# Kernel tuning notes

Measured on AMD Instinct MI355X. Metric: run time of the kernel, lower is better.

Reference implementation:

```python
import jax, jax.numpy as jnp
import numpy as np

HID = 128
NUM_LAYERS = 3
B = 256
ND, ED, SD = 16384, 65536, 131072
NP_, EP, SP = 131072, 524288, 524288


def setup_inputs():
    key = jax.random.key(0)
    ks = jax.random.split(key, 40)
    r = lambda i, sh: jax.random.normal(ks[i], sh, jnp.float32) * 0.05
    ri = lambda i, sh, hi: jax.random.randint(ks[i], sh, 0, hi, jnp.int32)
    return {
        'drug_x': r(0, (ND, 78)),
        'prot_x': r(1, (NP_, 70)),
        'd_feature': r(2, (B, HID)),
        'p_feature': r(3, (B, HID)),
        'drug_edge_index': ri(4, (2, ED), ND),
        'drug_batch': jnp.sort(ri(5, (ND,), B)),
        'drug_sub_node': ri(6, (SD,), ND),
        'drug_sub_ind': ri(7, (SD,), ND),
        'prot_edge_index': ri(8, (2, EP), NP_),
        'prot_batch': jnp.sort(ri(9, (NP_,), B)),
        'prot_sub_node': ri(10, (SP,), NP_),
        'prot_sub_ind': ri(11, (SP,), NP_),
        'enc_Wd': r(12, (78, HID)), 'enc_bd': r(13, (HID,)),
        'enc_Wp': r(14, (70, HID)), 'enc_bp': r(15, (HID,)),
        'convW_d': r(16, (NUM_LAYERS, HID, HID)), 'convb_d': r(17, (NUM_LAYERS, HID)),
        'convW_p': r(18, (NUM_LAYERS, HID, HID)), 'convb_p': r(19, (NUM_LAYERS, HID)),
        'bng_d': jnp.ones((NUM_LAYERS, HID), jnp.float32), 'bnb_d': jnp.zeros((NUM_LAYERS, HID), jnp.float32),
        'bng_p': jnp.ones((NUM_LAYERS, HID), jnp.float32), 'bnb_p': jnp.zeros((NUM_LAYERS, HID), jnp.float32),
        'vn_emb_d': r(20, (HID,)), 'vn_emb_p': r(21, (HID,)),
        'vnW_d': r(22, (NUM_LAYERS - 1, HID, HID)), 'vnb_d': r(23, (NUM_LAYERS - 1, HID)),
        'vnW_p': r(24, (NUM_LAYERS - 1, HID, HID)), 'vnb_p': r(25, (NUM_LAYERS - 1, HID)),
        'mlpd1_W': r(26, (2 * HID, HID)), 'mlpd1_b': r(27, (HID,)),
        'mlpd1_g': jnp.ones((HID,), jnp.float32), 'mlpd1_be': jnp.zeros((HID,), jnp.float32),
        'mlpp1_W': r(28, (2 * HID, HID)), 'mlpp1_b': r(29, (HID,)),
        'mlpp1_g': jnp.ones((HID,), jnp.float32), 'mlpp1_be': jnp.zeros((HID,), jnp.float32),
    }


def _bn(x, g, b):
    # training-mode batch norm (batch statistics)
    m = jnp.mean(x, 0)
    v = jnp.var(x, 0)
    return (x - m) * jax.lax.rsqrt(v + 1e-5) * g + b


def _seg_mean(x, ids, n):
    s = jax.ops.segment_sum(x, ids, num_segments=n)
    c = jax.ops.segment_sum(jnp.ones((x.shape[0],), x.dtype), ids, num_segments=n)
    return s / jnp.maximum(c, 1.0)[:, None]


def _gcn(h, W, b, ei, n):
    # PyG GCNConv: sym-normalized A+I, then linear
    src, dst = ei[0], ei[1]
    hw = h @ W
    deg = jax.ops.segment_sum(jnp.ones((src.shape[0],), h.dtype), dst, num_segments=n) + 1.0
    nrm = jax.lax.rsqrt(deg)
    msg = hw[src] * (nrm[src] * nrm[dst])[:, None]  # [E, HID]
    return jax.ops.segment_sum(msg, dst, num_segments=n) + hw * (nrm * nrm)[:, None] + b


def _forward(fl, ints):
    (drug_x, prot_x, d_feature, p_feature, enc_Wd, enc_bd, enc_Wp, enc_bp,
     convW_d, convb_d, convW_p, convb_p, bng_d, bnb_d, bng_p, bnb_p,
     vn_emb_d, vn_emb_p, vnW_d, vnb_d, vnW_p, vnb_p,
     mlpd1_W, mlpd1_b, mlpd1_g, mlpd1_be, mlpp1_W, mlpp1_b, mlpp1_g, mlpp1_be) = fl
    (d_ei, d_batch, d_sn, d_si, p_ei, p_batch, p_sn, p_si) = ints
    Nd, Npn = drug_x.shape[0], prot_x.shape[0]
    Bn = d_feature.shape[0]
    hd = drug_x @ enc_Wd + enc_bd
    hp = prot_x @ enc_Wp + enc_bp
    # virtual node init: learned embedding + pretrained fingerprint feature
    vx_d = vn_emb_d[None, :] + d_feature  # [B, HID]
    vx_p = vn_emb_p[None, :] + p_feature
    for i in range(NUM_LAYERS):
        # virtual-node broadcast -> GCN -> BN -> ReLU (dropout off / eval)
        hd = _gcn(hd + vx_d[d_batch], convW_d[i], convb_d[i], d_ei, Nd)
        hp = _gcn(hp + vx_p[p_batch], convW_p[i], convb_p[i], p_ei, Npn)
        hd = jax.nn.relu(_bn(hd, bng_d[i], bnb_d[i]))
        hp = jax.nn.relu(_bn(hp, bng_p[i], bnb_p[i]))
        # k-hop subgraph structure extraction (scatter_mean back to nodes)
        hd_struct = _seg_mean(hd[d_sn], d_si, Nd)
        hp_struct = _seg_mean(hp[p_sn], p_si, Npn)
        if i < NUM_LAYERS - 1:
            vx_d = vx_d + jax.nn.relu((jax.ops.segment_sum(hd_struct, d_batch, num_segments=Bn) + vx_d) @ vnW_d[i] + vnb_d[i])
            vx_p = vx_p + jax.nn.relu((jax.ops.segment_sum(hp_struct, p_batch, num_segments=Bn) + vx_p) @ vnW_p[i] + vnb_p[i])
    # cross-modal sync: broadcast pooled drug info onto protein nodes & vice versa
    sync_drug = hp_struct + _seg_mean(hd_struct, d_batch, Bn)[p_batch]  # [Np, HID]
    sync_prot = hd_struct + _seg_mean(hp_struct, p_batch, Bn)[d_batch]  # [Nd, HID]
    final_drug = _bn(jnp.concatenate([_seg_mean(sync_prot, d_batch, Bn), d_feature], 1) @ mlpd1_W + mlpd1_b, mlpd1_g, mlpd1_be)
    final_prot = _bn(jnp.concatenate([_seg_mean(sync_drug, p_batch, Bn), p_feature], 1) @ mlpp1_W + mlpp1_b, mlpp1_g, mlpp1_be)
    return final_drug, final_prot


def reference(drug_x, prot_x, d_feature, p_feature, drug_edge_index, drug_batch,
              drug_sub_node, drug_sub_ind, prot_edge_index, prot_batch,
              prot_sub_node, prot_sub_ind, enc_Wd, enc_bd, enc_Wp, enc_bp,
              convW_d, convb_d, convW_p, convb_p, bng_d, bnb_d, bng_p, bnb_p,
              vn_emb_d, vn_emb_p, vnW_d, vnb_d, vnW_p, vnb_p,
              mlpd1_W, mlpd1_b, mlpd1_g, mlpd1_be, mlpp1_W, mlpp1_b, mlpp1_g, mlpp1_be):
    fl = (drug_x, prot_x, d_feature, p_feature, enc_Wd, enc_bd, enc_Wp, enc_bp,
          convW_d, convb_d, convW_p, convb_p, bng_d, bnb_d, bng_p, bnb_p,
          vn_emb_d, vn_emb_p, vnW_d, vnb_d, vnW_p, vnb_p,
          mlpd1_W, mlpd1_b, mlpd1_g, mlpd1_be, mlpp1_W, mlpp1_b, mlpp1_g, mlpp1_be)
    ints = (drug_edge_index, drug_batch, drug_sub_node, drug_sub_ind,
            prot_edge_index, prot_batch, prot_sub_node, prot_sub_ind)
    return _forward(fl, ints)
```

## Files before the change

### kernel.cpp

```cpp
#include <hip/hip_runtime.h>
#include <cstdint>
#include <cstddef>

#define HID 128

using bf16x8 = __attribute__((ext_vector_type(8))) short;
using f32x4v = __attribute__((ext_vector_type(4))) float;

static __device__ __forceinline__ unsigned short f2b(float x) {
  unsigned int u = __float_as_uint(x);
  unsigned int r = u + 0x7FFFu + ((u >> 16) & 1u);
  return (unsigned short)(r >> 16);
}
static __device__ __forceinline__ float b2f(unsigned short h) {
  return __uint_as_float(((unsigned int)h) << 16);
}

static __device__ __forceinline__ int lowerb(const int* __restrict__ a, int n, int v) {
  int lo = 0, hi = n;
  while (lo < hi) { int m = (lo + hi) >> 1; if (a[m] < v) lo = m + 1; else hi = m; }
  return lo;
}

__global__ void k_hist_all(const int* i0, int n0, int* c0, const int* i1, int n1, int* c1,
                           const int* i2, int n2, int* c2, const int* i3, int n3, int* c3) {
  const int seg = blockIdx.x & 3;
  const int lb = blockIdx.x >> 2;
  const int stride = (gridDim.x >> 2) * blockDim.x;
  const int start = lb * blockDim.x + threadIdx.x;
  const int* idx = seg == 0 ? i0 : seg == 1 ? i1 : seg == 2 ? i2 : i3;
  int* cnt = seg == 0 ? c0 : seg == 1 ? c1 : seg == 2 ? c2 : c3;
  const int n = seg == 0 ? n0 : seg == 1 ? n1 : seg == 2 ? n2 : n3;
  for (int i = start; i < n; i += stride) atomicAdd(&cnt[idx[i]], 1);
}

__global__ void k_nrm_nb(const int* __restrict__ deg_d, float* __restrict__ nrm_d, int ND,
                         const int* __restrict__ deg_p, float* __restrict__ nrm_p, int NP,
                         const int* __restrict__ d_batch, float* __restrict__ nb_d,
                         const int* __restrict__ p_batch, float* __restrict__ nb_p, int B) {
  const int stride = gridDim.x * blockDim.x;
  const int total = ND + NP + 2 * B;
  for (int i = blockIdx.x * blockDim.x + threadIdx.x; i < total; i += stride) {
    if (i < ND) nrm_d[i] = rsqrtf((float)deg_d[i] + 1.0f);
    else if (i < ND + NP) { const int j = i - ND; nrm_p[j] = rsqrtf((float)deg_p[j] + 1.0f); }
    else if (i < ND + NP + B) {
      const int b = i - ND - NP;
      nb_d[b] = (float)(lowerb(d_batch, ND, b + 1) - lowerb(d_batch, ND, b));
    } else {
      const int b = i - ND - NP - B;
      nb_p[b] = (float)(lowerb(p_batch, NP, b + 1) - lowerb(p_batch, NP, b));
    }
  }
}

__global__ __launch_bounds__(256)
void k_scan1_all(const int* c0, int* r0, int n0, int nb0,
                 const int* c1, int* r1, int n1, int nb1,
                 const int* c2, int* r2, int n2, int nb2,
                 const int* c3, int* r3, int n3, int nb3, int* aux) {
  __shared__ int sh[256];
  int b = blockIdx.x, seg = 0;
  if (b >= nb0) { b -= nb0; seg = 1; }
  if (seg == 1 && b >= nb1) { b -= nb1; seg = 2; }
  if (seg == 2 && b >= nb2) { b -= nb2; seg = 3; }
  const int* cnt = seg == 0 ? c0 : seg == 1 ? c1 : seg == 2 ? c2 : c3;
  int* row = seg == 0 ? r0 : seg == 1 ? r1 : seg == 2 ? r2 : r3;
  const int n = seg == 0 ? n0 : seg == 1 ? n1 : seg == 2 ? n2 : n3;
  const int tid = threadIdx.x;
  const int base = b * 1024 + tid * 4;
  int v0 = base + 0 < n ? cnt[base + 0] : 0;
  int v1 = base + 1 < n ? cnt[base + 1] : 0;
  int v2 = base + 2 < n ? cnt[base + 2] : 0;
  int v3 = base + 3 < n ? cnt[base + 3] : 0;
  const int s = v0 + v1 + v2 + v3;
  sh[tid] = s;
  __syncthreads();
  for (int o = 1; o < 256; o <<= 1) {
    const int t = (tid >= o) ? sh[tid - o] : 0;
    __syncthreads();
    sh[tid] += t;
    __syncthreads();
  }
  int excl = sh[tid] - s;
  if (tid == 255) aux[seg * 256 + b] = sh[255];
  if (base + 0 < n) row[base + 0] = excl; excl += v0;
  if (base + 1 < n) row[base + 1] = excl; excl += v1;
  if (base + 2 < n) row[base + 2] = excl; excl += v2;
  if (base + 3 < n) row[base + 3] = excl;
}

__global__ __launch_bounds__(256)
void k_scan2_all(int* aux, int nb0, int nb1, int nb2, int nb3) {
  __shared__ int sh[256];
  const int seg = blockIdx.x;
  const int nb = seg == 0 ? nb0 : seg == 1 ? nb1 : seg == 2 ? nb2 : nb3;
  int* a = aux + seg * 256;
  const int tid = threadIdx.x;
  const int v = tid < nb ? a[tid] : 0;
  sh[tid] = v;
  __syncthreads();
  for (int o = 1; o < 256; o <<= 1) {
    const int t = (tid >= o) ? sh[tid - o] : 0;
    __syncthreads();
    sh[tid] += t;
    __syncthreads();
  }
  if (tid < nb) a[tid] = sh[tid] - v;
}

__global__ __launch_bounds__(256)
void k_scan3_all(int* r0, int n0, int nb0, int t0, int* r1, int n1, int nb1, int t1,
                 int* r2, int n2, int nb2, int t2, int* r3, int n3, int nb3, int t3,
                 const int* aux) {
  int b = blockIdx.x, seg = 0;
  if (b >= nb0) { b -= nb0; seg = 1; }
  if (seg == 1 && b >= nb1) { b -= nb1; seg = 2; }
  if (seg == 2 && b >= nb2) { b -= nb2; seg = 3; }
  int* row = seg == 0 ? r0 : seg == 1 ? r1 : seg == 2 ? r2 : r3;
  const int n = seg == 0 ? n0 : seg == 1 ? n1 : seg == 2 ? n2 : n3;
  const int total = seg == 0 ? t0 : seg == 1 ? t1 : seg == 2 ? t2 : t3;
  const int add = aux[seg * 256 + b];
  const int base = b * 1024 + threadIdx.x * 4;
  #pragma unroll
  for (int k = 0; k < 4; ++k)
    if (base + k < n) row[base + k] += add;
  if (b == 0 && threadIdx.x == 0) row[n] = total;
}

__global__ void k_fill_all(const int* p_src, const int* p_dst, const int* rowE_p, int* curE_p,
                           int* colE_p, float* cofE_p, const float* nrm_p, int EP,
                           const int* d_src, const int* d_dst, const int* rowE_d, int* curE_d,
                           int* colE_d, float* cofE_d, const float* nrm_d, int ED,
                           const int* p_sn, const int* p_si, const int* rowS_p, int* curS_p,
                           int* colS_p, int SP,
                           const int* d_sn, const int* d_si, const int* rowS_d, int* curS_d,
                           int* colS_d, int SD) {
  const int seg = blockIdx.x & 3;
  const int lb = blockIdx.x >> 2;
  const int stride = (gridDim.x >> 2) * blockDim.x;
  const int start = lb * blockDim.x + threadIdx.x;
  if (seg == 0) {
    for (int e = start; e < EP; e += stride) {
      const int d = p_dst[e], s = p_src[e];
      const int pos = rowE_p[d] + atomicAdd(&curE_p[d], 1);
      colE_p[pos] = s;
      cofE_p[pos] = nrm_p[s] * nrm_p[d];
    }
  } else if (seg == 1) {
    for (int e = start; e < ED; e += stride) {
      const int d = d_dst[e], s = d_src[e];
      const int pos = rowE_d[d] + atomicAdd(&curE_d[d], 1);
      colE_d[pos] = s;
      cofE_d[pos] = nrm_d[s] * nrm_d[d];
    }
  } else if (seg == 2) {
    for (int j = start; j < SP; j += stride) {
      const int t = p_si[j];
      const int pos = rowS_p[t] + atomicAdd(&curS_p[t], 1);
      colS_p[pos] = p_sn[j];
    }
  } else {
    for (int j = start; j < SD; j += stride) {
      const int t = d_si[j];
      const int pos = rowS_d[t] + atomicAdd(&curS_d[t], 1);
      colS_d[pos] = d_sn[j];
    }
  }
}

__global__ void k_vx_init_both(const float* __restrict__ emb_d, const float* __restrict__ d_feat,
                               float* __restrict__ vx_d, const float* __restrict__ emb_p,
                               const float* __restrict__ p_feat, float* __restrict__ vx_p,
                               int half) {
  const int stride = gridDim.x * blockDim.x;
  for (int i = blockIdx.x * blockDim.x + threadIdx.x; i < 2 * half; i += stride) {
    if (i < half) vx_d[i] = emb_d[i & (HID - 1)] + d_feat[i];
    else { const int j = i - half; vx_p[j] = emb_p[j & (HID - 1)] + p_feat[j]; }
  }
}

__global__ __launch_bounds__(256)
void k_wcvt_all(const float* __restrict__ convW_d, const float* __restrict__ convW_p,
                const float* __restrict__ enc_Wd, const float* __restrict__ enc_Wp,
                unsigned short* __restrict__ WhiAll, unsigned short* __restrict__ WloAll) {
  const int seg = blockIdx.x >> 5;
  const int lb = blockIdx.x & 31;
  const float* W;
  int K;
  if (seg < 3) { W = convW_d + (size_t)seg * HID * HID; K = 128; }
  else if (seg < 6) { W = convW_p + (size_t)(seg - 3) * HID * HID; K = 128; }
  else if (seg == 6) { W = enc_Wd; K = 78; }
  else { W = enc_Wp; K = 70; }
  unsigned short* Whi = WhiAll + (size_t)seg * HID * HID;
  unsigned short* Wlo = WloAll + (size_t)seg * HID * HID;
  for (int i = lb * 256 + threadIdx.x; i < HID * HID; i += 32 * 256) {
    const int c = i >> 7, k = i & 127;
    const float v = (k < K) ? W[k * HID + c] : 0.f;
    const unsigned short hi = f2b(v);
    Whi[i] = hi;
    Wlo[i] = f2b(v - b2f(hi));
  }
}

__global__ void k_xcvt_both(const float* __restrict__ Xd, int Kd, unsigned short* __restrict__ Dhi,
                            unsigned short* __restrict__ Dlo, int totD,
                            const float* __restrict__ Xp, int Kp, unsigned short* __restrict__ Phi,
                            unsigned short* __restrict__ Plo, int totP) {
  const int stride = gridDim.x * blockDim.x;
  for (int i = blockIdx.x * blockDim.x + threadIdx.x; i < totD + totP; i += stride) {
    if (i < totD) {
      const int node = i >> 7, k = i & 127;
      const float v = (k < Kd) ? Xd[(size_t)node * Kd + k] : 0.f;
      const unsigned short hi = f2b(v);
      Dhi[i] = hi;
      Dlo[i] = f2b(v - b2f(hi));
    } else {
      const int j = i - totD;
      const int node = j >> 7, k = j & 127;
      const float v = (k < Kp) ? Xp[(size_t)node * Kp + k] : 0.f;
      const unsigned short hi = f2b(v);
      Phi[j] = hi;
      Plo[j] = f2b(v - b2f(hi));
    }
  }
}

template<bool ENC>
__global__ __launch_bounds__(256, 2)
void k_gemm_both(const unsigned short* __restrict__ Zhi0, const unsigned short* __restrict__ Zlo0,
                 const unsigned short* __restrict__ Whi0, const unsigned short* __restrict__ Wlo0,
                 const float* __restrict__ bias0, float* __restrict__ G0, int nbk0,
                 const unsigned short* __restrict__ Zhi1, const unsigned short* __restrict__ Zlo1,
                 const unsigned short* __restrict__ Whi1, const unsigned short* __restrict__ Wlo1,
                 const float* __restrict__ bias1, float* __restrict__ G1,
                 float* __restrict__ stats_sl) {
  __shared__ unsigned short Bt[128 * 132];
  __shared__ float lstats[256];
  const int bid = blockIdx.x;
  const bool isP = bid >= nbk0;
  const int lb = isP ? bid - nbk0 : bid;
  const unsigned short* Zhi = isP ? Zhi1 : Zhi0;
  const unsigned short* Zlo = isP ? Zlo1 : Zlo0;
  const unsigned short* Wthi = isP ? Whi1 : Whi0;
  const unsigned short* Wtlo = isP ? Wlo1 : Wlo0;
  const float* bias = isP ? bias1 : bias0;
  float* G = isP ? G1 : G0;

  const int tid = threadIdx.x;
  const int w = tid >> 6;
  const int l = tid & 63;
  const int l15 = l & 15;
  const int kb = l >> 4;

  for (int i = tid; i < 128 * 16; i += 256) {
    const int c = i >> 4, k8 = i & 15;
    *(bf16x8*)(&Bt[c * 132 + k8 * 8]) = *(const bf16x8*)(Wthi + (size_t)c * 128 + k8 * 8);
  }
  if constexpr (!ENC) lstats[tid] = 0.f;

  const int rbase = lb * 128 + w * 32 + l15;
  bf16x8 ahi[2][4], alo[2][4];
  #pragma unroll
  for (int rt = 0; rt < 2; ++rt)
    #pragma unroll
    for (int ks = 0; ks < 4; ++ks) {
      ahi[rt][ks] = *(const bf16x8*)(Zhi + (size_t)(rbase + rt * 16) * 128 + ks * 32 + kb * 8);
      alo[rt][ks] = *(const bf16x8*)(Zlo + (size_t)(rbase + rt * 16) * 128 + ks * 32 + kb * 8);
    }

  f32x4v acc[2][8];
  #pragma unroll
  for (int rt = 0; rt < 2; ++rt)
    #pragma unroll
    for (int ct = 0; ct < 8; ++ct)
      acc[rt][ct] = (f32x4v){0.f, 0.f, 0.f, 0.f};

  __syncthreads();
  #pragma unroll
  for (int ks = 0; ks < 4; ++ks) {
    #pragma unroll
    for (int ct = 0; ct < 8; ++ct) {
      const bf16x8 b = *(const bf16x8*)(&Bt[(ct * 16 + l15) * 132 + ks * 32 + kb * 8]);
      acc[0][ct] = __builtin_amdgcn_mfma_f32_16x16x32_bf16(ahi[0][ks], b, acc[0][ct], 0, 0, 0);
      acc[1][ct] = __builtin_amdgcn_mfma_f32_16x16x32_bf16(ahi[1][ks], b, acc[1][ct], 0, 0, 0);
      acc[0][ct] = __builtin_amdgcn_mfma_f32_16x16x32_bf16(alo[0][ks], b, acc[0][ct], 0, 0, 0);
      acc[1][ct] = __builtin_amdgcn_mfma_f32_16x16x32_bf16(alo[1][ks], b, acc[1][ct], 0, 0, 0);
    }
  }
  __syncthreads();

  for (int i = tid; i < 128 * 16; i += 256) {
    const int c = i >> 4, k8 = i & 15;
    *(bf16x8*)(&Bt[c * 132 + k8 * 8]) = *(const bf16x8*)(Wtlo + (size_t)c * 128 + k8 * 8);
  }
  __syncthreads();
  #pragma unroll
  for (int ks = 0; ks < 4; ++ks) {
    #pragma unroll
    for (int ct = 0; ct < 8; ++ct) {
      const bf16x8 b = *(const bf16x8*)(&Bt[(ct * 16 + l15) * 132 + ks * 32 + kb * 8]);
      acc[0][ct] = __builtin_amdgcn_mfma_f32_16x16x32_bf16(ahi[0][ks], b, acc[0][ct], 0, 0, 0);
      acc[1][ct] = __builtin_amdgcn_mfma_f32_16x16x32_bf16(ahi[1][ks], b, acc[1][ct], 0, 0, 0);
    }
  }

  float bb[8];
  if constexpr (ENC) {
    #pragma unroll
    for (int ct = 0; ct < 8; ++ct) bb[ct] = bias[ct * 16 + l15];
  }
  float csum[8], csq[8];
  #pragma unroll
  for (int ct = 0; ct < 8; ++ct) { csum[ct] = 0.f; csq[ct] = 0.f; }
  #pragma unroll
  for (int rt = 0; rt < 2; ++rt) {
    const size_t grow = (size_t)lb * 128 + w * 32 + rt * 16 + (l >> 4) * 4;
    #pragma unroll
    for (int j = 0; j < 4; ++j) {
      float* gr = G + (grow + j) * 128 + l15;
      #pragma unroll
      for (int ct = 0; ct < 8; ++ct) {
        float v = acc[rt][ct][j];
        if constexpr (ENC) v += bb[ct];
        gr[ct * 16] = v;
        if constexpr (!ENC) { csum[ct] += v; csq[ct] += v * v; }
      }
    }
  }
  if constexpr (!ENC) {
    #pragma unroll
    for (int ct = 0; ct < 8; ++ct) {
      csum[ct] += __shfl_xor(csum[ct], 16);
      csum[ct] += __shfl_xor(csum[ct], 32);
      csq[ct] += __shfl_xor(csq[ct], 16);
      csq[ct] += __shfl_xor(csq[ct], 32);
    }
    if (l < 16) {
      #pragma unroll
      for (int ct = 0; ct < 8; ++ct) {
        atomicAdd(&lstats[ct * 16 + l], csum[ct]);
        atomicAdd(&lstats[128 + ct * 16 + l], csq[ct]);
      }
    }
    __syncthreads();
    const int slice = (isP ? 32 : 0) + (lb & 31);
    atomicAdd(&stats_sl[(size_t)slice * 256 + tid], lstats[tid]);
  }
}

__global__ __launch_bounds__(128)
void k_bn_scale_both(float* __restrict__ stats_sl,
                     const float* g0, const float* b0, float invN0, float* scsh0,
                     const float* g1, const float* b1, float invN1, float* scsh1) {
  const int seg = blockIdx.x;
  float* base = stats_sl + (size_t)seg * 32 * 256;
  const float* g = seg ? g1 : g0;
  const float* bb = seg ? b1 : b0;
  const float invN = seg ? invN1 : invN0;
  float* scsh = seg ? scsh1 : scsh0;
  const int c = threadIdx.x;
  float s = 0.f, ss = 0.f;
  for (int k = 0; k < 32; ++k) {
    s += base[(size_t)k * 256 + c];
    ss += base[(size_t)k * 256 + 128 + c];
    base[(size_t)k * 256 + c] = 0.f;
    base[(size_t)k * 256 + 128 + c] = 0.f;
  }
  const float m = s * invN;
  const float var = ss * invN - m * m;
  const float sc = g[c] * rsqrtf(var + 1e-5f);
  scsh[c] = sc;
  scsh[HID + c] = bb[c] - m * sc;
}

template<bool HASF>
__global__ __launch_bounds__(256)
void k_agg_both(const int* rE0, const int* cE0, const float* wE0, const float* G0,
                const float* scsh0, const int* bat0, const float* vx0, const float* nrm0,
                unsigned short* Zhi0, unsigned short* Zlo0, int nbk0,
                const int* rE1, const int* cE1, const float* wE1, const float* G1,
                const float* scsh1, const int* bat1, const float* vx1, const float* nrm1,
                unsigned short* Zhi1, unsigned short* Zlo1) {
  const int bid = blockIdx.x;
  const bool isP = bid >= nbk0;
  const int lb = isP ? bid - nbk0 : bid;
  const int* rowp = isP ? rE1 : rE0;
  const int* colp = isP ? cE1 : cE0;
  const float* coefp = isP ? wE1 : wE0;
  const float* G = isP ? G1 : G0;
  const float* scsh = isP ? scsh1 : scsh0;
  const int* batch = isP ? bat1 : bat0;
  const float* vx = isP ? vx1 : vx0;
  const float* nrm = isP ? nrm1 : nrm0;
  unsigned short* Zhi = isP ? Zhi1 : Zhi0;
  unsigned short* Zlo = isP ? Zlo1 : Zlo0;

  const int tid = threadIdx.x;
  const int node = lb * 8 + (tid >> 5);
  const int c4 = tid & 31;
  float4 sc, shv;
  if constexpr (HASF) {
    sc = ((const float4*)scsh)[c4];
    shv = ((const float4*)(scsh + HID))[c4];
  }
  auto loadU = [&](int i) -> float4 {
    float4 v = *(const float4*)(G + (size_t)i * HID + c4 * 4);
    if constexpr (HASF) {
      v.x = fmaxf(v.x * sc.x + shv.x, 0.f);
      v.y = fmaxf(v.y * sc.y + shv.y, 0.f);
      v.z = fmaxf(v.z * sc.z + shv.z, 0.f);
      v.w = fmaxf(v.w * sc.w + shv.w, 0.f);
    }
    const float4 u = *(const float4*)(vx + (size_t)batch[i] * HID + c4 * 4);
    v.x += u.x; v.y += u.y; v.z += u.z; v.w += u.w;
    return v;
  };
  const int lo = rowp[node], hi = rowp[node + 1];
  const float nv = nrm[node];
  const float s2 = nv * nv;
  float4 acc = loadU(node);
  acc.x *= s2; acc.y *= s2; acc.z *= s2; acc.w *= s2;
  int e = lo;
  for (; e + 4 <= hi; e += 4) {
    const float w0 = coefp[e], w1 = coefp[e + 1], w2 = coefp[e + 2], w3 = coefp[e + 3];
    const float4 v0 = loadU(colp[e]);
    const float4 v1 = loadU(colp[e + 1]);
    const float4 v2 = loadU(colp[e + 2]);
    const float4 v3 = loadU(colp[e + 3]);
    acc.x += v0.x * w0 + v1.x * w1 + v2.x * w2 + v3.x * w3;
    acc.y += v0.y * w0 + v1.y * w1 + v2.y * w2 + v3.y * w3;
    acc.z += v0.z * w0 + v1.z * w1 + v2.z * w2 + v3.z * w3;
    acc.w += v0.w * w0 + v1.w * w1 + v2.w * w2 + v3.w * w3;
  }
  for (; e < hi; ++e) {
    const float w = coefp[e];
    const float4 v = loadU(colp[e]);
    acc.x += v.x * w; acc.y += v.y * w; acc.z += v.z * w; acc.w += v.w * w;
  }
  ushort4 h, lo4;
  h.x = f2b(acc.x); lo4.x = f2b(acc.x - b2f(h.x));
  h.y = f2b(acc.y); lo4.y = f2b(acc.y - b2f(h.y));
  h.z = f2b(acc.z); lo4.z = f2b(acc.z - b2f(h.z));
  h.w = f2b(acc.w); lo4.w = f2b(acc.w - b2f(h.w));
  *(ushort4*)(Zhi + (size_t)node * HID + c4 * 4) = h;
  *(ushort4*)(Zlo + (size_t)node * HID + c4 * 4) = lo4;
}

__global__ __launch_bounds__(256)
void k_sub_pool_both(const int* rS0, const int* cS0, const float* G0, const float* scsh0,
                     const int* bat0, float* sumS0, int nbk0,
                     const int* rS1, const int* cS1, const float* G1, const float* scsh1,
                     const int* bat1, float* sumS1) {
  __shared__ float sh[8][HID];
  __shared__ int batl[8];
  const int bid = blockIdx.x;
  const bool isP = bid >= nbk0;
  const int lb = isP ? bid - nbk0 : bid;
  const int* rowp = isP ? rS1 : rS0;
  const int* colp = isP ? cS1 : cS0;
  const float* G = isP ? G1 : G0;
  const float* scsh = isP ? scsh1 : scsh0;
  const int* batch = isP ? bat1 : bat0;
  float* sumS = isP ? sumS1 : sumS0;

  const int tid = threadIdx.x;
  const int grp = tid >> 5;
  const int node = lb * 8 + grp;
  const int c4 = tid & 31;
  const float4 sc = ((const float4*)scsh)[c4];
  const float4 shv = ((const float4*)(scsh + HID))[c4];
  const int lo = rowp[node], hi = rowp[node + 1];
  float4 acc = {0.f, 0.f, 0.f, 0.f};
  int e = lo;
  for (; e + 4 <= hi; e += 4) {
    const int i0 = colp[e], i1 = colp[e + 1], i2 = colp[e + 2], i3 = colp[e + 3];
    const float4 v0 = *(const float4*)(G + (size_t)i0 * HID + c4 * 4);
    const float4 v1 = *(const float4*)(G + (size_t)i1 * HID + c4 * 4);
    const float4 v2 = *(const float4*)(G + (size_t)i2 * HID + c4 * 4);
    const float4 v3 = *(const float4*)(G + (size_t)i3 * HID + c4 * 4);
    acc.x += fmaxf(v0.x * sc.x + shv.x, 0.f) + fmaxf(v1.x * sc.x + shv.x, 0.f)
           + fmaxf(v2.x * sc.x + shv.x, 0.f) + fmaxf(v3.x * sc.x + shv.x, 0.f);
    acc.y += fmaxf(v0.y * sc.y + shv.y, 0.f) + fmaxf(v1.y * sc.y + shv.y, 0.f)
           + fmaxf(v2.y * sc.y + shv.y, 0.f) + fmaxf(v3.y * sc.y + shv.y, 0.f);
    acc.z += fmaxf(v0.z * sc.z + shv.z, 0.f) + fmaxf(v1.z * sc.z + shv.z, 0.f)
           + fmaxf(v2.z * sc.z + shv.z, 0.f) + fmaxf(v3.z * sc.z + shv.z, 0.f);
    acc.w += fmaxf(v0.w * sc.w + shv.w, 0.f) + fmaxf(v1.w * sc.w + shv.w, 0.f)
           + fmaxf(v2.w * sc.w + shv.w, 0.f) + fmaxf(v3.w * sc.w + shv.w, 0.f);
  }
  for (; e < hi; ++e) {
    const float4 v = *(const float4*)(G + (size_t)colp[e] * HID + c4 * 4);
    acc.x += fmaxf(v.x * sc.x + shv.x, 0.f);
    acc.y += fmaxf(v.y * sc.y + shv.y, 0.f);
    acc.z += fmaxf(v.z * sc.z + shv.z, 0.f);
    acc.w += fmaxf(v.w * sc.w + shv.w, 0.f);
  }
  const float inv = 1.0f / fmaxf((float)(hi - lo), 1.0f);
  acc.x *= inv; acc.y *= inv; acc.z *= inv; acc.w *= inv;
  ((float4*)&sh[grp][0])[c4] = acc;
  if (tid < 8) batl[tid] = batch[lb * 8 + tid];
  __syncthreads();
  if (tid < HID) {
    int cur = batl[0];
    float a = 0.f;
    #pragma unroll
    for (int g = 0; g < 8; ++g) {
      if (batl[g] != cur) {
        atomicAdd(&sumS[(size_t)cur * HID + tid], a);
        a = 0.f;
        cur = batl[g];
      }
      a += sh[g][tid];
    }
    atomicAdd(&sumS[(size_t)cur * HID + tid], a);
  }
}

__global__ __launch_bounds__(128)
void k_vn_update_both(const float* ps0, float* vx0, const float* W0, const float* b0,
                      const float* ps1, float* vx1, const float* W1, const float* b1, int B) {
  const int gb = blockIdx.x;
  const bool isP = gb >= B;
  const int b = isP ? gb - B : gb;
  const float* pooledSum = isP ? ps1 : ps0;
  float* vx = isP ? vx1 : vx0;
  const float* W = isP ? W1 : W0;
  const float* bias = isP ? b1 : b0;
  const int c = threadIdx.x;
  __shared__ float xin[HID];
  xin[c] = pooledSum[(size_t)b * HID + c] + vx[(size_t)b * HID + c];
  __syncthreads();
  float acc = bias[c];
  #pragma unroll 8
  for (int k = 0; k < HID; k += 4) {
    const float4 x = *(const float4*)&xin[k];
    acc += x.x * W[k * HID + c] + x.y * W[(k + 1) * HID + c]
         + x.z * W[(k + 2) * HID + c] + x.w * W[(k + 3) * HID + c];
  }
  vx[(size_t)b * HID + c] += fmaxf(acc, 0.0f);
}

__global__ __launch_bounds__(128)
void k_final_A(const float* __restrict__ sum_Sd, const float* __restrict__ sum_Sp,
               const float* __restrict__ nb_d, const float* __restrict__ nb_p,
               float* __restrict__ A_d, float* __restrict__ A_p) {
  const int b = blockIdx.x, c = threadIdx.x;
  const float nd = nb_d[b], np_ = nb_p[b];
  const float md = sum_Sd[(size_t)b * HID + c] / fmaxf(nd, 1.f);
  const float mp = sum_Sp[(size_t)b * HID + c] / fmaxf(np_, 1.f);
  A_d[(size_t)b * HID + c] = md + (nd > 0.f ? mp : 0.f);
  A_p[(size_t)b * HID + c] = mp + (np_ > 0.f ? md : 0.f);
}

__global__ __launch_bounds__(128)
void k_final_mlp_both(const float* A0, const float* f0, const float* W0, const float* b0,
                      const float* A1, const float* f1, const float* W1, const float* b1,
                      float* __restrict__ fpre, int B) {
  const int gb = blockIdx.x;
  const bool isP = gb >= B;
  const int b = isP ? gb - B : gb;
  const float* A = isP ? A1 : A0;
  const float* feat = isP ? f1 : f0;
  const float* W = isP ? W1 : W0;
  const float* bias = isP ? b1 : b0;
  const int c = threadIdx.x;
  __shared__ float xin[2 * HID];
  xin[c] = A[(size_t)b * HID + c];
  xin[HID + c] = feat[(size_t)b * HID + c];
  __syncthreads();
  float acc = bias[c];
  #pragma unroll 8
  for (int k = 0; k < 2 * HID; k += 4) {
    const float4 x = *(const float4*)&xin[k];
    acc += x.x * W[k * HID + c] + x.y * W[(k + 1) * HID + c]
         + x.z * W[(k + 2) * HID + c] + x.w * W[(k + 3) * HID + c];
  }
  fpre[(size_t)gb * HID + c] = acc;
}

__global__ __launch_bounds__(256)
void k_bn_stats_both(const float* __restrict__ fpre, float* __restrict__ statsF, int B) {
  __shared__ float sh[2][256];
  const int seg = blockIdx.x >= 128 ? 1 : 0;
  const int lb = blockIdx.x - seg * 128;
  const float* X = fpre + (size_t)seg * B * HID;
  float* stats = statsF + seg * 256;
  const int tid = threadIdx.x;
  const int c = tid & (HID - 1);
  const int half = tid >> 7;
  float s = 0.f, ss = 0.f;
  for (int r = lb * 2 + half; r < B; r += 256) {
    const float v = X[(size_t)r * HID + c];
    s += v; ss += v * v;
  }
  sh[0][tid] = s; sh[1][tid] = ss;
  __syncthreads();
  if (tid < HID) {
    atomicAdd(&stats[c], sh[0][tid] + sh[0][tid + 128]);
    atomicAdd(&stats[HID + c], sh[1][tid] + sh[1][tid + 128]);
  }
}

__global__ void k_bn_apply_both(const float* __restrict__ fpre, float* __restrict__ out,
                                const float* __restrict__ statsF,
                                const float* g0, const float* b0,
                                const float* g1, const float* b1, int B, float invN) {
  const int stride = gridDim.x * blockDim.x;
  const int n4 = 2 * B * 32;
  for (int i = blockIdx.x * blockDim.x + threadIdx.x; i < n4; i += stride) {
    const int seg = i >= B * 32 ? 1 : 0;
    const int c4 = i & 31;
    const float* stats = statsF + seg * 256;
    const float4 m4 = ((const float4*)stats)[c4];
    const float4 q4 = ((const float4*)stats)[32 + c4];
    const float4 g4 = ((const float4*)(seg ? g1 : g0))[c4];
    const float4 b4 = ((const float4*)(seg ? b1 : b0))[c4];
    float4 v = ((const float4*)fpre)[i];
    float m, va;
    m = m4.x * invN; va = q4.x * invN - m * m; v.x = (v.x - m) * rsqrtf(va + 1e-5f) * g4.x + b4.x;
    m = m4.y * invN; va = q4.y * invN - m * m; v.y = (v.y - m) * rsqrtf(va + 1e-5f) * g4.y + b4.y;
    m = m4.z * invN; va = q4.z * invN - m * m; v.z = (v.z - m) * rsqrtf(va + 1e-5f) * g4.z + b4.z;
    m = m4.w * invN; va = q4.w * invN - m * m; v.w = (v.w - m) * rsqrtf(va + 1e-5f) * g4.w + b4.w;
    ((float4*)out)[i] = v;
  }
}

extern "C" void kernel_launch(void* const* d_in, const int* in_sizes, int n_in,
                              void* d_out, int out_size, void* d_ws, size_t ws_size,
                              hipStream_t stream) {
  const float* drug_x   = (const float*)d_in[0];
  const float* prot_x   = (const float*)d_in[1];
  const float* d_feat   = (const float*)d_in[2];
  const float* p_feat   = (const float*)d_in[3];
  const int*   d_ei     = (const int*)d_in[4];
  const int*   d_batch  = (const int*)d_in[5];
  const int*   d_sn     = (const int*)d_in[6];
  const int*   d_si     = (const int*)d_in[7];
  const int*   p_ei     = (const int*)d_in[8];
  const int*   p_batch  = (const int*)d_in[9];
  const int*   p_sn     = (const int*)d_in[10];
  const int*   p_si     = (const int*)d_in[11];
  const float* enc_Wd   = (const float*)d_in[12];
  const float* enc_bd   = (const float*)d_in[13];
  const float* enc_Wp   = (const float*)d_in[14];
  const float* enc_bp   = (const float*)d_in[15];
  const float* convW_d  = (const float*)d_in[16];
  const float* convW_p  = (const float*)d_in[18];
  const float* bng_d    = (const float*)d_in[20];
  const float* bnb_d    = (const float*)d_in[21];
  const float* bng_p    = (const float*)d_in[22];
  const float* bnb_p    = (const float*)d_in[23];
  const float* vn_emb_d = (const float*)d_in[24];
  const float* vn_emb_p = (const float*)d_in[25];
  const float* vnW_d    = (const float*)d_in[26];
  const float* vnb_d    = (const float*)d_in[27];
  const float* vnW_p    = (const float*)d_in[28];
  const float* vnb_p    = (const float*)d_in[29];
  const float* mlpd1_W  = (const float*)d_in[30];
  const float* mlpd1_b  = (const float*)d_in[31];
  const float* mlpd1_g  = (const float*)d_in[32];
  const float* mlpd1_be = (const float*)d_in[33];
  const float* mlpp1_W  = (const float*)d_in[34];
  const float* mlpp1_b  = (const float*)d_in[35];
  const float* mlpp1_g  = (const float*)d_in[36];
  const float* mlpp1_be = (const float*)d_in[37];

  const int ND = in_sizes[5];
  const int ED = in_sizes[4] / 2;
  const int SD = in_sizes[6];
  const int NP = in_sizes[9];
  const int EP = in_sizes[8] / 2;
  const int SP = in_sizes[10];
  const int B  = in_sizes[2] / HID;
  (void)n_in; (void)out_size; (void)ws_size;

  char* wsb = (char*)d_ws;
  size_t off = 0;
  auto alloc = [&](size_t bytes) -> void* {
    void* p = (void*)(wsb + off);
    off = (off + bytes + 255) & ~(size_t)255;
    return p;
  };
  float* Gp = (float*)alloc((size_t)NP * HID * 4);
  unsigned short* Zhi_p = (unsigned short*)alloc((size_t)NP * HID * 2);
  unsigned short* Zlo_p = (unsigned short*)alloc((size_t)NP * HID * 2);
  float* Gd = (float*)alloc((size_t)ND * HID * 4);
  unsigned short* Zhi_d = (unsigned short*)alloc((size_t)ND * HID * 2);
  unsigned short* Zlo_d = (unsigned short*)alloc((size_t)ND * HID * 2);
  unsigned short* WhiAll = (unsigned short*)alloc((size_t)8 * HID * HID * 2);
  unsigned short* WloAll = (unsigned short*)alloc((size_t)8 * HID * HID * 2);
  float* nrm_p = (float*)alloc((size_t)NP * 4);
  float* nrm_d = (float*)alloc((size_t)ND * 4);
  int* rowE_p = (int*)alloc((size_t)(NP + 1) * 4);
  int* rowE_d = (int*)alloc((size_t)(ND + 1) * 4);
  int* rowS_p = (int*)alloc((size_t)(NP + 1) * 4);
  int* rowS_d = (int*)alloc((size_t)(ND + 1) * 4);
  int* colE_p = (int*)alloc((size_t)EP * 4);
  float* cofE_p = (float*)alloc((size_t)EP * 4);
  int* colE_d = (int*)alloc((size_t)ED * 4);
  float* cofE_d = (float*)alloc((size_t)ED * 4);
  int* colS_p = (int*)alloc((size_t)SP * 4);
  int* colS_d = (int*)alloc((size_t)SD * 4);
  int* aux    = (int*)alloc(4 * 256 * 4);
  float* vx_d  = (float*)alloc((size_t)B * HID * 4);
  float* vx_p  = (float*)alloc((size_t)B * HID * 4);
  float* sum_Sd = (float*)alloc((size_t)B * HID * 4);
  float* sum_Sp = (float*)alloc((size_t)B * HID * 4);
  float* A_d   = (float*)alloc((size_t)B * HID * 4);
  float* A_p   = (float*)alloc((size_t)B * HID * 4);
  float* nb_d  = (float*)alloc((size_t)B * 4);
  float* nb_p  = (float*)alloc((size_t)B * 4);
  float* scsh_d = (float*)alloc(2 * HID * 4);
  float* scsh_p = (float*)alloc(2 * HID * 4);
  float* fpre  = (float*)alloc((size_t)2 * B * HID * 4);
  float* statsF = (float*)alloc(2 * 256 * 4);
  const size_t zstart = off;
  int* deg_p  = (int*)alloc((size_t)NP * 4);
  int* deg_d  = (int*)alloc((size_t)ND * 4);
  int* scnt_p = (int*)alloc((size_t)NP * 4);
  int* scnt_d = (int*)alloc((size_t)ND * 4);
  int* curE_p = (int*)alloc((size_t)NP * 4);
  int* curE_d = (int*)alloc((size_t)ND * 4);
  int* curS_p = (int*)alloc((size_t)NP * 4);
  int* curS_d = (int*)alloc((size_t)ND * 4);
  float* stats_sl = (float*)alloc((size_t)64 * 256 * 4);
  const size_t zend = off;

  const int* d_src = d_ei;  const int* d_dst = d_ei + ED;
  const int* p_src = p_ei;  const int* p_dst = p_ei + EP;

  hipMemsetAsync(wsb + zstart, 0, zend - zstart, stream);
  k_hist_all<<<4096, 256, 0, stream>>>(p_dst, EP, deg_p, d_dst, ED, deg_d,
                                       p_si, SP, scnt_p, d_si, SD, scnt_d);
  k_nrm_nb<<<1024, 256, 0, stream>>>(deg_d, nrm_d, ND, deg_p, nrm_p, NP,
                                     d_batch, nb_d, p_batch, nb_p, B);
  const int nbP = (NP + 1023) / 1024, nbD = (ND + 1023) / 1024;
  k_scan1_all<<<2 * nbP + 2 * nbD, 256, 0, stream>>>(
      deg_p, rowE_p, NP, nbP, deg_d, rowE_d, ND, nbD,
      scnt_p, rowS_p, NP, nbP, scnt_d, rowS_d, ND, nbD, aux);
  k_scan2_all<<<4, 256, 0, stream>>>(aux, nbP, nbD, nbP, nbD);
  k_scan3_all<<<2 * nbP + 2 * nbD, 256, 0, stream>>>(
      rowE_p, NP, nbP, EP, rowE_d, ND, nbD, ED,
      rowS_p, NP, nbP, SP, rowS_d, ND, nbD, SD, aux);
  k_fill_all<<<4096, 256, 0, stream>>>(
      p_src, p_dst, rowE_p, curE_p, colE_p, cofE_p, nrm_p, EP,
      d_src, d_dst, rowE_d, curE_d, colE_d, cofE_d, nrm_d, ED,
      p_sn, p_si, rowS_p, curS_p, colS_p, SP,
      d_sn, d_si, rowS_d, curS_d, colS_d, SD);

  k_wcvt_all<<<256, 256, 0, stream>>>(convW_d, convW_p, enc_Wd, enc_Wp, WhiAll, WloAll);
  k_xcvt_both<<<4096, 256, 0, stream>>>(drug_x, 78, Zhi_d, Zlo_d, ND * HID,
                                        prot_x, 70, Zhi_p, Zlo_p, NP * HID);
  k_gemm_both<true><<<ND / 128 + NP / 128, 256, 0, stream>>>(
      Zhi_d, Zlo_d, WhiAll + (size_t)6 * HID * HID, WloAll + (size_t)6 * HID * HID,
      enc_bd, Gd, ND / 128,
      Zhi_p, Zlo_p, WhiAll + (size_t)7 * HID * HID, WloAll + (size_t)7 * HID * HID,
      enc_bp, Gp, nullptr);
  k_vx_init_both<<<128, 256, 0, stream>>>(vn_emb_d, d_feat, vx_d, vn_emb_p, p_feat, vx_p, B * HID);

  for (int l = 0; l < 3; ++l) {
    if (l == 0)
      k_agg_both<false><<<ND / 8 + NP / 8, 256, 0, stream>>>(
          rowE_d, colE_d, cofE_d, Gd, nullptr, d_batch, vx_d, nrm_d, Zhi_d, Zlo_d, ND / 8,
          rowE_p, colE_p, cofE_p, Gp, nullptr, p_batch, vx_p, nrm_p, Zhi_p, Zlo_p);
    else
      k_agg_both<true><<<ND / 8 + NP / 8, 256, 0, stream>>>(
          rowE_d, colE_d, cofE_d, Gd, scsh_d, d_batch, vx_d, nrm_d, Zhi_d, Zlo_d, ND / 8,
          rowE_p, colE_p, cofE_p, Gp, scsh_p, p_batch, vx_p, nrm_p, Zhi_p, Zlo_p);
    k_gemm_both<false><<<ND / 128 + NP / 128, 256, 0, stream>>>(
        Zhi_d, Zlo_d, WhiAll + (size_t)l * HID * HID, WloAll + (size_t)l * HID * HID,
        nullptr, Gd, ND / 128,
        Zhi_p, Zlo_p, WhiAll + (size_t)(3 + l) * HID * HID, WloAll + (size_t)(3 + l) * HID * HID,
        nullptr, Gp, stats_sl);
    k_bn_scale_both<<<2, 128, 0, stream>>>(stats_sl,
        bng_d + l * HID, bnb_d + l * HID, 1.0f / (float)ND, scsh_d,
        bng_p + l * HID, bnb_p + l * HID, 1.0f / (float)NP, scsh_p);
    hipMemsetAsync(sum_Sd, 0, (size_t)2 * B * HID * 4, stream);
    k_sub_pool_both<<<ND / 8 + NP / 8, 256, 0, stream>>>(
        rowS_d, colS_d, Gd, scsh_d, d_batch, sum_Sd, ND / 8,
        rowS_p, colS_p, Gp, scsh_p, p_batch, sum_Sp);
    if (l < 2)
      k_vn_update_both<<<2 * B, 128, 0, stream>>>(
          sum_Sd, vx_d, vnW_d + (size_t)l * HID * HID, vnb_d + l * HID,
          sum_Sp, vx_p, vnW_p + (size_t)l * HID * HID, vnb_p + l * HID, B);
  }

  k_final_A<<<B, 128, 0, stream>>>(sum_Sd, sum_Sp, nb_d, nb_p, A_d, A_p);
  k_final_mlp_both<<<2 * B, 128, 0, stream>>>(A_d, d_feat, mlpd1_W, mlpd1_b,
                                              A_p, p_feat, mlpp1_W, mlpp1_b, fpre, B);
  hipMemsetAsync(statsF, 0, 2 * 256 * 4, stream);
  k_bn_stats_both<<<256, 256, 0, stream>>>(fpre, statsF, B);
  k_bn_apply_both<<<128, 256, 0, stream>>>(fpre, (float*)d_out, statsF,
                                           mlpd1_g, mlpd1_be, mlpp1_g, mlpp1_be,
                                           B, 1.0f / (float)B);
}
```

Measured before the change: 719.7 us.

## Fuse preprocessing kernels, compute edge coefficients on the fly, fold memset into BN

Merges the histogram, input conversion, weight conversion and virtual-node init kernels into one launch, split by block index. Drops the per-edge coefficient arrays and instead computes nrm[src]*nrm[dst] inside aggregation, removing the float scatter writes in the fill step. Moves the per-layer memset of the pooling sums into the BN-scale kernel. Together these cut launch count and memory traffic, at the cost of an extra gather of nrm per edge in each aggregation pass.

```diff
diff --git a/kernel.cpp b/kernel.cpp
--- a/kernel.cpp
+++ b/kernel.cpp
@@ -3,6 +3,8 @@
 #include <cstddef>
 
 #define HID 128
+#define HB 1024
+#define XB 2048
 
 using bf16x8 = __attribute__((ext_vector_type(8))) short;
 using f32x4v = __attribute__((ext_vector_type(4))) float;
@@ -22,22 +24,74 @@
   return lo;
 }
 
-__global__ void k_hist_all(const int* i0, int n0, int* c0, const int* i1, int n1, int* c1,
-                           const int* i2, int n2, int* c2, const int* i3, int n3, int* c3) {
-  const int seg = blockIdx.x & 3;
-  const int lb = blockIdx.x >> 2;
-  const int stride = (gridDim.x >> 2) * blockDim.x;
-  const int start = lb * blockDim.x + threadIdx.x;
-  const int* idx = seg == 0 ? i0 : seg == 1 ? i1 : seg == 2 ? i2 : i3;
-  int* cnt = seg == 0 ? c0 : seg == 1 ? c1 : seg == 2 ? c2 : c3;
-  const int n = seg == 0 ? n0 : seg == 1 ? n1 : seg == 2 ? n2 : n3;
-  for (int i = start; i < n; i += stride) atomicAdd(&cnt[idx[i]], 1);
-}
-
-__global__ void k_nrm_nb(const int* __restrict__ deg_d, float* __restrict__ nrm_d, int ND,
-                         const int* __restrict__ deg_p, float* __restrict__ nrm_p, int NP,
-                         const int* __restrict__ d_batch, float* __restrict__ nb_d,
-                         const int* __restrict__ p_batch, float* __restrict__ nb_p, int B) {
+__global__ __launch_bounds__(256)
+void k_prep1(const int* p_dst, int EP, int* deg_p, const int* d_dst, int ED, int* deg_d,
+             const int* p_si, int SP, int* scnt_p, const int* d_si, int SD, int* scnt_d,
+             const float* Xd, int Kd, unsigned short* Dhi, unsigned short* Dlo, int totD,
+             const float* Xp, int Kp, unsigned short* Phi, unsigned short* Plo, int totP,
+             const float* convW_d, const float* convW_p,
+             const float* enc_Wd, const float* enc_Wp,
+             unsigned short* WhiAll, unsigned short* WloAll,
+             const float* emb_d, const float* d_feat, float* vx_d,
+             const float* emb_p, const float* p_feat, float* vx_p, int vhalf) {
+  const int b = blockIdx.x;
+  const int tid = threadIdx.x;
+  if (b < 4 * HB) {
+    const int seg = b & 3, lb = b >> 2;
+    const int stride = HB * 256;
+    const int* idx = seg == 0 ? p_dst : seg == 1 ? d_dst : seg == 2 ? p_si : d_si;
+    int* cnt = seg == 0 ? deg_p : seg == 1 ? deg_d : seg == 2 ? scnt_p : scnt_d;
+    const int n = seg == 0 ? EP : seg == 1 ? ED : seg == 2 ? SP : SD;
+    for (int i = lb * 256 + tid; i < n; i += stride) atomicAdd(&cnt[idx[i]], 1);
+  } else if (b < 4 * HB + XB) {
+    const int lb = b - 4 * HB;
+    for (int i = lb * 256 + tid; i < totD + totP; i += XB * 256) {
+      if (i < totD) {
+        const int node = i >> 7, k = i & 127;
+        const float v = (k < Kd) ? Xd[(size_t)node * Kd + k] : 0.f;
+        const unsigned short hi = f2b(v);
+        Dhi[i] = hi;
+        Dlo[i] = f2b(v - b2f(hi));
+      } else {
+        const int j = i - totD;
+        const int node = j >> 7, k = j & 127;
+        const float v = (k < Kp) ? Xp[(size_t)node * Kp + k] : 0.f;
+        const unsigned short hi = f2b(v);
+        Phi[j] = hi;
+        Plo[j] = f2b(v - b2f(hi));
+      }
+    }
+  } else if (b < 4 * HB + XB + 256) {
+    const int lb = b - (4 * HB + XB);
+    const int seg = lb >> 5;
+    const float* W;
+    int K;
+    if (seg < 3) { W = convW_d + (size_t)seg * HID * HID; K = 128; }
+    else if (seg < 6) { W = convW_p + (size_t)(seg - 3) * HID * HID; K = 128; }
+    else if (seg == 6) { W = enc_Wd; K = 78; }
+    else { W = enc_Wp; K = 70; }
+    unsigned short* Whi = WhiAll + (size_t)seg * HID * HID;
+    unsigned short* Wlo = WloAll + (size_t)seg * HID * HID;
+    for (int i = (lb & 31) * 256 + tid; i < HID * HID; i += 32 * 256) {
+      const int c = i >> 7, k = i & 127;
+      const float v = (k < K) ? W[k * HID + c] : 0.f;
+      const unsigned short hi = f2b(v);
+      Whi[i] = hi;
+      Wlo[i] = f2b(v - b2f(hi));
+    }
+  } else {
+    const int lb = b - (4 * HB + XB + 256);
+    for (int i = lb * 256 + tid; i < 2 * vhalf; i += 128 * 256) {
+      if (i < vhalf) vx_d[i] = emb_d[i & (HID - 1)] + d_feat[i];
+      else { const int j = i - vhalf; vx_p[j] = emb_p[j & (HID - 1)] + p_feat[j]; }
+    }
+  }
+}
+
+__global__ void k_nrm_nb(const int* deg_d, float* nrm_d, int ND,
+                         const int* deg_p, float* nrm_p, int NP,
+                         const int* d_batch, float* nb_d,
+                         const int* p_batch, float* nb_p, int B) {
   const int stride = gridDim.x * blockDim.x;
   const int total = ND + NP + 2 * B;
   for (int i = blockIdx.x * blockDim.x + threadIdx.x; i < total; i += stride) {
@@ -128,9 +182,9 @@
 }
 
 __global__ void k_fill_all(const int* p_src, const int* p_dst, const int* rowE_p, int* curE_p,
-                           int* colE_p, float* cofE_p, const float* nrm_p, int EP,
+                           int* colE_p, int EP,
                            const int* d_src, const int* d_dst, const int* rowE_d, int* curE_d,
-                           int* colE_d, float* cofE_d, const float* nrm_d, int ED,
+                           int* colE_d, int ED,
                            const int* p_sn, const int* p_si, const int* rowS_p, int* curS_p,
                            int* colS_p, int SP,
                            const int* d_sn, const int* d_si, const int* rowS_d, int* curS_d,
@@ -141,86 +195,23 @@
   const int start = lb * blockDim.x + threadIdx.x;
   if (seg == 0) {
     for (int e = start; e < EP; e += stride) {
-      const int d = p_dst[e], s = p_src[e];
-      const int pos = rowE_p[d] + atomicAdd(&curE_p[d], 1);
-      colE_p[pos] = s;
-      cofE_p[pos] = nrm_p[s] * nrm_p[d];
+      const int d = p_dst[e];
+      colE_p[rowE_p[d] + atomicAdd(&curE_p[d], 1)] = p_src[e];
     }
   } else if (seg == 1) {
     for (int e = start; e < ED; e += stride) {
-      const int d = d_dst[e], s = d_src[e];
-      const int pos = rowE_d[d] + atomicAdd(&curE_d[d], 1);
-      colE_d[pos] = s;
-      cofE_d[pos] = nrm_d[s] * nrm_d[d];
+      const int d = d_dst[e];
+      colE_d[rowE_d[d] + atomicAdd(&curE_d[d], 1)] = d_src[e];
     }
   } else if (seg == 2) {
     for (int j = start; j < SP; j += stride) {
       const int t = p_si[j];
-      const int pos = rowS_p[t] + atomicAdd(&curS_p[t], 1);
-      colS_p[pos] = p_sn[j];
+      colS_p[rowS_p[t] + atomicAdd(&curS_p[t], 1)] = p_sn[j];
     }
   } else {
     for (int j = start; j < SD; j += stride) {
       const int t = d_si[j];
-      const int pos = rowS_d[t] + atomicAdd(&curS_d[t], 1);
-      colS_d[pos] = d_sn[j];
-    }
-  }
-}
-
-__global__ void k_vx_init_both(const float* __restrict__ emb_d, const float* __restrict__ d_feat,
-                               float* __restrict__ vx_d, const float* __restrict__ emb_p,
-                               const float* __restrict__ p_feat, float* __restrict__ vx_p,
-                               int half) {
-  const int stride = gridDim.x * blockDim.x;
-  for (int i = blockIdx.x * blockDim.x + threadIdx.x; i < 2 * half; i += stride) {
-    if (i < half) vx_d[i] = emb_d[i & (HID - 1)] + d_feat[i];
-    else { const int j = i - half; vx_p[j] = emb_p[j & (HID - 1)] + p_feat[j]; }
-  }
-}
-
-__global__ __launch_bounds__(256)
-void k_wcvt_all(const float* __restrict__ convW_d, const float* __restrict__ convW_p,
-                const float* __restrict__ enc_Wd, const float* __restrict__ enc_Wp,
-                unsigned short* __restrict__ WhiAll, unsigned short* __restrict__ WloAll) {
-  const int seg = blockIdx.x >> 5;
-  const int lb = blockIdx.x & 31;
-  const float* W;
-  int K;
-  if (seg < 3) { W = convW_d + (size_t)seg * HID * HID; K = 128; }
-  else if (seg < 6) { W = convW_p + (size_t)(seg - 3) * HID * HID; K = 128; }
-  else if (seg == 6) { W = enc_Wd; K = 78; }
-  else { W = enc_Wp; K = 70; }
-  unsigned short* Whi = WhiAll + (size_t)seg * HID * HID;
-  unsigned short* Wlo = WloAll + (size_t)seg * HID * HID;
-  for (int i = lb * 256 + threadIdx.x; i < HID * HID; i += 32 * 256) {
-    const int c = i >> 7, k = i & 127;
-    const float v = (k < K) ? W[k * HID + c] : 0.f;
-    const unsigned short hi = f2b(v);
-    Whi[i] = hi;
-    Wlo[i] = f2b(v - b2f(hi));
-  }
-}
-
-__global__ void k_xcvt_both(const float* __restrict__ Xd, int Kd, unsigned short* __restrict__ Dhi,
-                            unsigned short* __restrict__ Dlo, int totD,
-                            const float* __restrict__ Xp, int Kp, unsigned short* __restrict__ Phi,
-                            unsigned short* __restrict__ Plo, int totP) {
-  const int stride = gridDim.x * blockDim.x;
-  for (int i = blockIdx.x * blockDim.x + threadIdx.x; i < totD + totP; i += stride) {
-    if (i < totD) {
-      const int node = i >> 7, k = i & 127;
-      const float v = (k < Kd) ? Xd[(size_t)node * Kd + k] : 0.f;
-      const unsigned short hi = f2b(v);
-      Dhi[i] = hi;
-      Dlo[i] = f2b(v - b2f(hi));
-    } else {
-      const int j = i - totD;
-      const int node = j >> 7, k = j & 127;
-      const float v = (k < Kp) ? Xp[(size_t)node * Kp + k] : 0.f;
-      const unsigned short hi = f2b(v);
-      Phi[j] = hi;
-      Plo[j] = f2b(v - b2f(hi));
+      colS_d[rowS_d[t] + atomicAdd(&curS_d[t], 1)] = d_sn[j];
     }
   }
 }
@@ -350,14 +341,16 @@
 
 __global__ __launch_bounds__(128)
 void k_bn_scale_both(float* __restrict__ stats_sl,
-                     const float* g0, const float* b0, float invN0, float* scsh0,
-                     const float* g1, const float* b1, float invN1, float* scsh1) {
+                     const float* g0, const float* b0, float invN0, float* scsh0, float* zero0,
+                     const float* g1, const float* b1, float invN1, float* scsh1, float* zero1,
+                     int zn4) {
   const int seg = blockIdx.x;
   float* base = stats_sl + (size_t)seg * 32 * 256;
   const float* g = seg ? g1 : g0;
   const float* bb = seg ? b1 : b0;
   const float invN = seg ? invN1 : invN0;
   float* scsh = seg ? scsh1 : scsh0;
+  float* zero = seg ? zero1 : zero0;
   const int c = threadIdx.x;
   float s = 0.f, ss = 0.f;
   for (int k = 0; k < 32; ++k) {
@@ -371,14 +364,16 @@
   const float sc = g[c] * rsqrtf(var + 1e-5f);
   scsh[c] = sc;
   scsh[HID + c] = bb[c] - m * sc;
+  const float4 z = {0.f, 0.f, 0.f, 0.f};
+  for (int i = c; i < zn4; i += 128) ((float4*)zero)[i] = z;
 }
 
 template<bool HASF>
 __global__ __launch_bounds__(256)
-void k_agg_both(const int* rE0, const int* cE0, const float* wE0, const float* G0,
+void k_agg_both(const int* rE0, const int* cE0, const float* G0,
                 const float* scsh0, const int* bat0, const float* vx0, const float* nrm0,
                 unsigned short* Zhi0, unsigned short* Zlo0, int nbk0,
-                const int* rE1, const int* cE1, const float* wE1, const float* G1,
+                const int* rE1, const int* cE1, const float* G1,
                 const float* scsh1, const int* bat1, const float* vx1, const float* nrm1,
                 unsigned short* Zhi1, unsigned short* Zlo1) {
   const int bid = blockIdx.x;
@@ -386,7 +381,6 @@
   const int lb = isP ? bid - nbk0 : bid;
   const int* rowp = isP ? rE1 : rE0;
   const int* colp = isP ? cE1 : cE0;
-  const float* coefp = isP ? wE1 : wE0;
   const float* G = isP ? G1 : G0;
   const float* scsh = isP ? scsh1 : scsh0;
   const int* batch = isP ? bat1 : bat0;
@@ -422,19 +416,21 @@
   acc.x *= s2; acc.y *= s2; acc.z *= s2; acc.w *= s2;
   int e = lo;
   for (; e + 4 <= hi; e += 4) {
-    const float w0 = coefp[e], w1 = coefp[e + 1], w2 = coefp[e + 2], w3 = coefp[e + 3];
-    const float4 v0 = loadU(colp[e]);
-    const float4 v1 = loadU(colp[e + 1]);
-    const float4 v2 = loadU(colp[e + 2]);
-    const float4 v3 = loadU(colp[e + 3]);
+    const int i0 = colp[e], i1 = colp[e + 1], i2 = colp[e + 2], i3 = colp[e + 3];
+    const float w0 = nrm[i0] * nv, w1 = nrm[i1] * nv, w2 = nrm[i2] * nv, w3 = nrm[i3] * nv;
+    const float4 v0 = loadU(i0);
+    const float4 v1 = loadU(i1);
+    const float4 v2 = loadU(i2);
+    const float4 v3 = loadU(i3);
     acc.x += v0.x * w0 + v1.x * w1 + v2.x * w2 + v3.x * w3;
     acc.y += v0.y * w0 + v1.y * w1 + v2.y * w2 + v3.y * w3;
     acc.z += v0.z * w0 + v1.z * w1 + v2.z * w2 + v3.z * w3;
     acc.w += v0.w * w0 + v1.w * w1 + v2.w * w2 + v3.w * w3;
   }
   for (; e < hi; ++e) {
-    const float w = coefp[e];
-    const float4 v = loadU(colp[e]);
+    const int i0 = colp[e];
+    const float w = nrm[i0] * nv;
+    const float4 v = loadU(i0);
     acc.x += v.x * w; acc.y += v.y * w; acc.z += v.z * w; acc.w += v.w * w;
   }
   ushort4 h, lo4;
@@ -695,9 +691,7 @@
   int* rowS_p = (int*)alloc((size_t)(NP + 1) * 4);
   int* rowS_d = (int*)alloc((size_t)(ND + 1) * 4);
   int* colE_p = (int*)alloc((size_t)EP * 4);
-  float* cofE_p = (float*)alloc((size_t)EP * 4);
   int* colE_d = (int*)alloc((size_t)ED * 4);
-  float* cofE_d = (float*)alloc((size_t)ED * 4);
   int* colS_p = (int*)alloc((size_t)SP * 4);
   int* colS_d = (int*)alloc((size_t)SD * 4);
   int* aux    = (int*)alloc(4 * 256 * 4);
@@ -729,8 +723,11 @@
   const int* p_src = p_ei;  const int* p_dst = p_ei + EP;
 
   hipMemsetAsync(wsb + zstart, 0, zend - zstart, stream);
-  k_hist_all<<<4096, 256, 0, stream>>>(p_dst, EP, deg_p, d_dst, ED, deg_d,
-                                       p_si, SP, scnt_p, d_si, SD, scnt_d);
+  k_prep1<<<4 * HB + XB + 256 + 128, 256, 0, stream>>>(
+      p_dst, EP, deg_p, d_dst, ED, deg_d, p_si, SP, scnt_p, d_si, SD, scnt_d,
+      drug_x, 78, Zhi_d, Zlo_d, ND * HID, prot_x, 70, Zhi_p, Zlo_p, NP * HID,
+      convW_d, convW_p, enc_Wd, enc_Wp, WhiAll, WloAll,
+      vn_emb_d, d_feat, vx_d, vn_emb_p, p_feat, vx_p, B * HID);
   k_nrm_nb<<<1024, 256, 0, stream>>>(deg_d, nrm_d, ND, deg_p, nrm_p, NP,
                                      d_batch, nb_d, p_batch, nb_p, B);
   const int nbP = (NP + 1023) / 1024, nbD = (ND + 1023) / 1024;
@@ -742,39 +739,35 @@
       rowE_p, NP, nbP, EP, rowE_d, ND, nbD, ED,
       rowS_p, NP, nbP, SP, rowS_d, ND, nbD, SD, aux);
   k_fill_all<<<4096, 256, 0, stream>>>(
-      p_src, p_dst, rowE_p, curE_p, colE_p, cofE_p, nrm_p, EP,
-      d_src, d_dst, rowE_d, curE_d, colE_d, cofE_d, nrm_d, ED,
+      p_src, p_dst, rowE_p, curE_p, colE_p, EP,
+      d_src, d_dst, rowE_d, curE_d, colE_d, ED,
       p_sn, p_si, rowS_p, curS_p, colS_p, SP,
       d_sn, d_si, rowS_d, curS_d, colS_d, SD);
 
-  k_wcvt_all<<<256, 256, 0, stream>>>(convW_d, convW_p, enc_Wd, enc_Wp, WhiAll, WloAll);
-  k_xcvt_both<<<4096, 256, 0, stream>>>(drug_x, 78, Zhi_d, Zlo_d, ND * HID,
-                                        prot_x, 70, Zhi_p, Zlo_p, NP * HID);
   k_gemm_both<true><<<ND / 128 + NP / 128, 256, 0, stream>>>(
       Zhi_d, Zlo_d, WhiAll + (size_t)6 * HID * HID, WloAll + (size_t)6 * HID * HID,
       enc_bd, Gd, ND / 128,
       Zhi_p, Zlo_p, WhiAll + (size_t)7 * HID * HID, WloAll + (size_t)7 * HID * HID,
       enc_bp, Gp, nullptr);
-  k_vx_init_both<<<128, 256, 0, stream>>>(vn_emb_d, d_feat, vx_d, vn_emb_p, p_feat, vx_p, B * HID);
 
   for (int l = 0; l < 3; ++l) {
     if (l == 0)
       k_agg_both<false><<<ND / 8 + NP / 8, 256, 0, stream>>>(
-          rowE_d, colE_d, cofE_d, Gd, nullptr, d_batch, vx_d, nrm_d, Zhi_d, Zlo_d, ND / 8,
-          rowE_p, colE_p, cofE_p, Gp, nullptr, p_batch, vx_p, nrm_p, Zhi_p, Zlo_p);
+          rowE_d, colE_d, Gd, nullptr, d_batch, vx_d, nrm_d, Zhi_d, Zlo_d, ND / 8,
+          rowE_p, colE_p, Gp, nullptr, p_batch, vx_p, nrm_p, Zhi_p, Zlo_p);
     else
       k_agg_both<true><<<ND / 8 + NP / 8, 256, 0, stream>>>(
-          rowE_d, colE_d, cofE_d, Gd, scsh_d, d_batch, vx_d, nrm_d, Zhi_d, Zlo_d, ND / 8,
-          rowE_p, colE_p, cofE_p, Gp, scsh_p, p_batch, vx_p, nrm_p, Zhi_p, Zlo_p);
+          rowE_d, colE_d, Gd, scsh_d, d_batch, vx_d, nrm_d, Zhi_d, Zlo_d, ND / 8,
+          rowE_p, colE_p, Gp, scsh_p, p_batch, vx_p, nrm_p, Zhi_p, Zlo_p);
     k_gemm_both<false><<<ND / 128 + NP / 128, 256, 0, stream>>>(
         Zhi_d, Zlo_d, WhiAll + (size_t)l * HID * HID, WloAll + (size_t)l * HID * HID,
         nullptr, Gd, ND / 128,
         Zhi_p, Zlo_p, WhiAll + (size_t)(3 + l) * HID * HID, WloAll + (size_t)(3 + l) * HID * HID,
         nullptr, Gp, stats_sl);
     k_bn_scale_both<<<2, 128, 0, stream>>>(stats_sl,
-        bng_d + l * HID, bnb_d + l * HID, 1.0f / (float)ND, scsh_d,
-        bng_p + l * HID, bnb_p + l * HID, 1.0f / (float)NP, scsh_p);
-    hipMemsetAsync(sum_Sd, 0, (size_t)2 * B * HID * 4, stream);
+        bng_d + l * HID, bnb_d + l * HID, 1.0f / (float)ND, scsh_d, sum_Sd,
+        bng_p + l * HID, bnb_p + l * HID, 1.0f / (float)NP, scsh_p, sum_Sp,
+        B * HID / 4);
     k_sub_pool_both<<<ND / 8 + NP / 8, 256, 0, stream>>>(
         rowS_d, colS_d, Gd, scsh_d, d_batch, sum_Sd, ND / 8,
         rowS_p, colS_p, Gp, scsh_p, p_batch, sum_Sp);
```

After: 709.1 us. Within noise of the previous version (-1.5%).
